# Performance work log

Hardware: AMD Instinct MI355X
Metric: run time of the kernel (lower is better)

Reference implementation:

```python
import jax, jax.numpy as jnp
import numpy as np

WIN = (16, 9, 9)
WIN_SIZE = WIN[0] * WIN[1] * WIN[2]  # 1296
EPS = float(np.e ** -15)             # ~3.06e-7, matches np.power(np.e, -15)


def setup_inputs() -> dict:
    key = jax.random.key(0)
    k1, k2 = jax.random.split(key)
    shape = (2, 1, 96, 192, 192)  # [B, 1, D, H, W]
    I = jax.random.normal(k1, shape, dtype=jnp.float32)
    J = jax.random.normal(k2, shape, dtype=jnp.float32)
    return {"I": I, "J": J}


def _box_sums(tmp):
    # Grouped conv3d with an all-ones [5,1,16,9,9] kernel: per-channel sliding
    k = jnp.ones((5, 1) + WIN, dtype=tmp.dtype)
    return jax.lax.conv_general_dilated(
        tmp, k,
        window_strides=(1, 1, 1),
        padding=[(0, 0), (WIN[1] // 2, WIN[1] // 2), (WIN[2] // 2, WIN[2] // 2)],
        feature_group_count=5,
        dimension_numbers=("NCDHW", "OIDHW", "NCDHW"),
    )


def reference(I, J):
    # I, J: [B, 1, D, H, W]
    tmp = jnp.concatenate([I, J, I * I, J * J, I * J], axis=1)  # [B,5,D,H,W]
    sums = _box_sums(tmp)  # [B, 5, D-15, H, W]
    I_sum, J_sum = sums[:, 0], sums[:, 1]
    I2_sum, J2_sum, IJ_sum = sums[:, 2], sums[:, 3], sums[:, 4]

    u_I = I_sum / WIN_SIZE
    u_J = J_sum / WIN_SIZE

    cross = IJ_sum - u_J * I_sum - u_I * J_sum + u_I * u_J * WIN_SIZE
    I_var = I2_sum - 2.0 * u_I * I_sum + u_I * u_I * WIN_SIZE
    J_var = J2_sum - 2.0 * u_J * J_sum + u_J * u_J * WIN_SIZE

    nz = (I_var * J_var) > EPS  # bool_non_zero; where false, substitute 1.0
    cross = jnp.where(nz, cross, 1.0)
    I_var = jnp.where(nz, I_var, 1.0)
    J_var = jnp.where(nz, J_var, 1.0)

    cc = cross * cross / (I_var * J_var + EPS)  # [B, D-15, H, W]
    loss = -1.0 * jnp.mean(cc, axis=(1, 2, 3)) + 1.0  # [B]
    return loss, cc
```

## Files before the change

### kernel.cpp

```cpp
#include <hip/hip_runtime.h>


constexpr int N = 2, D = 96, H = 192, W = 192;
constexpr int OD = 81;
constexpr int KD = 16;
constexpr int HWp = H * W;
constexpr float INV_WIN = 1.0f / 1296.0f;
constexpr float EPS_NZ = 3.0590232050182579e-07f;
constexpr int CH = 24;
constexpr int ODPB = 14;

__device__ __forceinline__ unsigned bf16rne(float f) {
  unsigned u = __float_as_uint(f);
  return (u + 0x7fffu + ((u >> 16) & 1u)) >> 16;
}
__device__ __forceinline__ float bf16tof(unsigned h) {
  return __uint_as_float(h << 16);
}

__global__ __launch_bounds__(192)
void k_dw(const float* __restrict__ I, const float* __restrict__ J,
          unsigned* __restrict__ ws, int od0, int c, int odcStride) {
  const int h = blockIdx.x;
  const int n = blockIdx.z;
  const int os = od0 + blockIdx.y * ODPB;
  int oe = od0 + c; if (os + ODPB < oe) oe = os + ODPB;
  if (os >= oe) return;
  const int w = threadIdx.x;

  __shared__ float4 x4[2][W + 8];
  __shared__ float  x1[2][W + 8];
  __shared__ float4 a4[2][W + 8];
  __shared__ float  a1[2][W + 8];

  if (w < 4) {
    x4[0][w] = make_float4(0.f,0.f,0.f,0.f); x1[0][w] = 0.f;
    x4[1][w] = make_float4(0.f,0.f,0.f,0.f); x1[1][w] = 0.f;
  }
  if (w >= W - 4) {
    x4[0][w + 8] = make_float4(0.f,0.f,0.f,0.f); x1[0][w + 8] = 0.f;
    x4[1][w + 8] = make_float4(0.f,0.f,0.f,0.f); x1[1][w + 8] = 0.f;
  }
  __syncthreads();

  const size_t colBase = ((size_t)n * D * H + h) * (size_t)W + w;
  const float* Ip = I + colBase;
  const float* Jp = J + colBase;
  unsigned* wbase = ws + ((size_t)n * odcStride * HWp + (size_t)h * W + w) * 3;

  int pe = -1;
  if (w < 3) pe = w + 1;
  else if (w >= W - 3) pe = w + 7;

  const int dEnd = oe + KD - 1;
  float sI = 0.f, sJ = 0.f, sII = 0.f, sJJ = 0.f, sIJ = 0.f;
  float ivN = Ip[(size_t)os * HWp];
  float jvN = Jp[(size_t)os * HWp];
  float ioN = 0.f, joN = 0.f;

  for (int d = os; d < dEnd; ++d) {
    const float iv = ivN, jv = jvN;
    const float io = ioN, jo = joN;
    const int dn = d + 1;
    if (dn < dEnd) {
      ivN = Ip[(size_t)dn * HWp];
      jvN = Jp[(size_t)dn * HWp];
      if (dn >= os + KD - 1) {
        const int odn = dn - (KD - 1);
        ioN = Ip[(size_t)odn * HWp];
        joN = Jp[(size_t)odn * HWp];
      }
    }
    sI += iv; sJ += jv;
    sII += iv * iv; sJJ += jv * jv; sIJ += iv * jv;
    if (d >= os + KD - 1) {
      const int od = d - (KD - 1);
      const int b = d & 1;
      const int p = 4 + w;
      x4[b][p] = make_float4(sI, sJ, sII, sJJ); x1[b][p] = sIJ;
      asm volatile("s_waitcnt lgkmcnt(0)" ::: "memory");
      __builtin_amdgcn_s_barrier();
      {
        float4 m0 = x4[b][p - 1], m1 = x4[b][p], m2 = x4[b][p + 1];
        a4[b][p] = make_float4(m0.x + m1.x + m2.x, m0.y + m1.y + m2.y,
                               m0.z + m1.z + m2.z, m0.w + m1.w + m2.w);
        a1[b][p] = x1[b][p - 1] + x1[b][p] + x1[b][p + 1];
        if (pe >= 0) {
          float4 e0 = x4[b][pe - 1], e1 = x4[b][pe], e2 = x4[b][pe + 1];
          a4[b][pe] = make_float4(e0.x + e1.x + e2.x, e0.y + e1.y + e2.y,
                                  e0.z + e1.z + e2.z, e0.w + e1.w + e2.w);
          a1[b][pe] = x1[b][pe - 1] + x1[b][pe] + x1[b][pe + 1];
        }
      }
      asm volatile("s_waitcnt lgkmcnt(0)" ::: "memory");
      __builtin_amdgcn_s_barrier();
      float4 b0 = a4[b][p - 3], b1 = a4[b][p], b2 = a4[b][p + 3];
      const float r0 = b0.x + b1.x + b2.x;
      const float r1 = b0.y + b1.y + b2.y;
      const float r2 = b0.z + b1.z + b2.z;
      const float r3 = b0.w + b1.w + b2.w;
      const float r4 = a1[b][p - 3] + a1[b][p] + a1[b][p + 3];
      unsigned* o = wbase + (size_t)(od - od0) * HWp * 3;
      uint3 v = make_uint3(bf16rne(r0) | (bf16rne(r1) << 16),
                           bf16rne(r2) | (bf16rne(r3) << 16),
                           bf16rne(r4));
      *(uint3*)o = v;
      sI -= io; sJ -= jo;
      sII -= io * io; sJJ -= jo * jo; sIJ -= io * jo;
    }
  }
}

__global__ __launch_bounds__(192)
void k_hcc(const unsigned* __restrict__ ws, float* __restrict__ cc,
           float* __restrict__ acc, int od0, int odcStride) {
  const int odi = blockIdx.x;
  const int od = od0 + odi;
  const int h0 = blockIdx.y * CH;
  const int n = blockIdx.z;
  const int w = threadIdx.x;
  const unsigned* base =
      ws + ((size_t)n * odcStride * HWp + (size_t)odi * HWp + w) * 3;
  float* ccp = cc + ((size_t)n * OD + od) * (size_t)HWp + w;

  float s0 = 0.f, s1 = 0.f, s2 = 0.f, s3 = 0.f, s4 = 0.f;
  float lsum = 0.f;
  uint3 hist[8];
  const uint3 z3 = make_uint3(0u, 0u, 0u);

  uint3 vN = z3;
  {
    const int hin = h0 - 4;
    if (hin >= 0) vN = *(const uint3*)(base + (size_t)hin * W * 3);
  }
#pragma unroll
  for (int t = 0; t < CH + 8; ++t) {
    const uint3 v = vN;
    if (t + 1 < CH + 8) {
      const int hn = h0 - 4 + t + 1;
      vN = (hn >= 0 && hn < H) ? *(const uint3*)(base + (size_t)hn * W * 3) : z3;
    }
    s0 += bf16tof(v.x & 0xffffu); s1 += bf16tof(v.x >> 16);
    s2 += bf16tof(v.y & 0xffffu); s3 += bf16tof(v.y >> 16);
    s4 += bf16tof(v.z & 0xffffu);
    if (t >= 8) {
      const int h = h0 + t - 8;
      const float cross = s4 - s0 * s1 * INV_WIN;
      const float vI = s2 - s0 * s0 * INV_WIN;
      const float vJ = s3 - s1 * s1 * INV_WIN;
      const float prod = vI * vJ;
      const float c = (prod > EPS_NZ) ? (cross * cross) / (prod + EPS_NZ)
                                      : 1.0f / (1.0f + EPS_NZ);
      ccp[(size_t)h * W] = c;
      lsum += c;
      const uint3 q = hist[t & 7];
      s0 -= bf16tof(q.x & 0xffffu); s1 -= bf16tof(q.x >> 16);
      s2 -= bf16tof(q.y & 0xffffu); s3 -= bf16tof(q.y >> 16);
      s4 -= bf16tof(q.z & 0xffffu);
    }
    hist[t & 7] = v;
  }
  __shared__ float red[3];
#pragma unroll
  for (int off = 32; off > 0; off >>= 1) lsum += __shfl_xor(lsum, off, 64);
  if ((threadIdx.x & 63) == 0) red[threadIdx.x >> 6] = lsum;
  __syncthreads();
  if (threadIdx.x == 0) atomicAdd(acc + n, red[0] + red[1] + red[2]);
}

__global__ void k_fin(const float* __restrict__ acc, float* __restrict__ out) {
  if (threadIdx.x < N)
    out[threadIdx.x] = 1.0f - acc[threadIdx.x] * (1.0f / 2985984.0f);
}

extern "C" void kernel_launch(void* const* d_in, const int* in_sizes, int n_in,
                              void* d_out, int out_size, void* d_ws,
                              size_t ws_size, hipStream_t stream) {
  const float* I = (const float*)d_in[0];
  const float* J = (const float*)d_in[1];
  float* out = (float*)d_out;
  float* acc = (float*)d_ws;
  unsigned* planes = (unsigned*)((char*)d_ws + 256);

  hipMemsetAsync(d_ws, 0, 2 * sizeof(float), stream);

  const size_t perOdPerN = (size_t)HWp * 12;
  size_t avail = (ws_size > 256) ? (ws_size - 256) : 0;
  long long odcMax = (long long)(avail / (2 * perOdPerN));
  if (odcMax < 1) odcMax = 1;
  if (odcMax > OD) odcMax = OD;
  const int odc = (int)odcMax;

  float* ccOut = out + 2;
  for (int od0 = 0; od0 < OD; od0 += odc) {
    const int c = (odc < OD - od0) ? odc : (OD - od0);
    const int S = (c + ODPB - 1) / ODPB;
    hipLaunchKernelGGL(k_dw, dim3(H, S, N), dim3(192), 0, stream,
                       I, J, planes, od0, c, odc);
    hipLaunchKernelGGL(k_hcc, dim3(c, H / CH, N), dim3(192), 0, stream,
                       planes, ccOut, acc, od0, odc);
  }
  hipLaunchKernelGGL(k_fin, dim3(1), dim3(64), 0, stream, acc, out);
}
```

Baseline: 73.29 us.

## Process two H rows per block and prefetch depth loads two steps ahead

The depth/width box-sum kernel now handles two adjacent H rows per block, so each barrier pair is shared across two rows and the grid is halved. It separates the 15-plane warm-up from the steady-state loop and uses a double-buffered register prefetch of entering and leaving planes two output depths ahead, to hide global load latency. The cost is more registers and shared memory per block and fewer blocks in flight, which may reduce occupancy.

```diff
diff --git a/kernel.cpp b/kernel.cpp
--- a/kernel.cpp
+++ b/kernel.cpp
@@ -21,94 +21,123 @@
 __global__ __launch_bounds__(192)
 void k_dw(const float* __restrict__ I, const float* __restrict__ J,
           unsigned* __restrict__ ws, int od0, int c, int odcStride) {
-  const int h = blockIdx.x;
+  const int hA = 2 * blockIdx.x, hB = hA + 1;
   const int n = blockIdx.z;
   const int os = od0 + blockIdx.y * ODPB;
   int oe = od0 + c; if (os + ODPB < oe) oe = os + ODPB;
   if (os >= oe) return;
   const int w = threadIdx.x;
 
-  __shared__ float4 x4[2][W + 8];
-  __shared__ float  x1[2][W + 8];
-  __shared__ float4 a4[2][W + 8];
-  __shared__ float  a1[2][W + 8];
+  __shared__ float4 xA4[W + 8]; __shared__ float xA1[W + 8];
+  __shared__ float4 xB4[W + 8]; __shared__ float xB1[W + 8];
+  __shared__ float4 aA4[W + 8]; __shared__ float aA1[W + 8];
+  __shared__ float4 aB4[W + 8]; __shared__ float aB1[W + 8];
 
   if (w < 4) {
-    x4[0][w] = make_float4(0.f,0.f,0.f,0.f); x1[0][w] = 0.f;
-    x4[1][w] = make_float4(0.f,0.f,0.f,0.f); x1[1][w] = 0.f;
+    xA4[w] = make_float4(0.f,0.f,0.f,0.f); xA1[w] = 0.f;
+    xB4[w] = make_float4(0.f,0.f,0.f,0.f); xB1[w] = 0.f;
   }
   if (w >= W - 4) {
-    x4[0][w + 8] = make_float4(0.f,0.f,0.f,0.f); x1[0][w + 8] = 0.f;
-    x4[1][w + 8] = make_float4(0.f,0.f,0.f,0.f); x1[1][w + 8] = 0.f;
+    xA4[w + 8] = make_float4(0.f,0.f,0.f,0.f); xA1[w + 8] = 0.f;
+    xB4[w + 8] = make_float4(0.f,0.f,0.f,0.f); xB1[w + 8] = 0.f;
   }
   __syncthreads();
 
-  const size_t colBase = ((size_t)n * D * H + h) * (size_t)W + w;
-  const float* Ip = I + colBase;
-  const float* Jp = J + colBase;
-  unsigned* wbase = ws + ((size_t)n * odcStride * HWp + (size_t)h * W + w) * 3;
+  const size_t baseA = ((size_t)n * D * H + hA) * (size_t)W + w;
+  const float* IpA = I + baseA;
+  const float* JpA = J + baseA;
+  const float* IpB = IpA + W;
+  const float* JpB = JpA + W;
+  unsigned* wbA = ws + ((size_t)n * odcStride * HWp + (size_t)hA * W + w) * 3;
+  unsigned* wbB = wbA + (size_t)W * 3;
 
   int pe = -1;
   if (w < 3) pe = w + 1;
   else if (w >= W - 3) pe = w + 7;
-
-  const int dEnd = oe + KD - 1;
-  float sI = 0.f, sJ = 0.f, sII = 0.f, sJJ = 0.f, sIJ = 0.f;
-  float ivN = Ip[(size_t)os * HWp];
-  float jvN = Jp[(size_t)os * HWp];
-  float ioN = 0.f, joN = 0.f;
-
-  for (int d = os; d < dEnd; ++d) {
-    const float iv = ivN, jv = jvN;
-    const float io = ioN, jo = joN;
-    const int dn = d + 1;
-    if (dn < dEnd) {
-      ivN = Ip[(size_t)dn * HWp];
-      jvN = Jp[(size_t)dn * HWp];
-      if (dn >= os + KD - 1) {
-        const int odn = dn - (KD - 1);
-        ioN = Ip[(size_t)odn * HWp];
-        joN = Jp[(size_t)odn * HWp];
-      }
+  const int p = 4 + w;
+
+  float sIA=0.f,sJA=0.f,sIIA=0.f,sJJA=0.f,sIJA=0.f;
+  float sIB=0.f,sJB=0.f,sIIB=0.f,sJJB=0.f,sIJB=0.f;
+  for (int d = os; d < os + KD - 1; ++d) {
+    const float ia = IpA[(size_t)d * HWp], ja = JpA[(size_t)d * HWp];
+    const float ib = IpB[(size_t)d * HWp], jb = JpB[(size_t)d * HWp];
+    sIA += ia; sJA += ja; sIIA += ia*ia; sJJA += ja*ja; sIJA += ia*ja;
+    sIB += ib; sJB += jb; sIIB += ib*ib; sJJB += jb*jb; sIJB += ib*jb;
+  }
+
+#define ISSUE(eIA,eJA,lIA,lJA,eIB,eJB,lIB,lJB, ODX)                          \
+  { const int _o = (ODX);                                                    \
+    eIA = IpA[(size_t)(_o + KD - 1) * HWp];                                  \
+    eJA = JpA[(size_t)(_o + KD - 1) * HWp];                                  \
+    lIA = IpA[(size_t)_o * HWp];                                             \
+    lJA = JpA[(size_t)_o * HWp];                                             \
+    eIB = IpB[(size_t)(_o + KD - 1) * HWp];                                  \
+    eJB = JpB[(size_t)(_o + KD - 1) * HWp];                                  \
+    lIB = IpB[(size_t)_o * HWp];                                             \
+    lJB = JpB[(size_t)_o * HWp]; }
+
+#define COMPUTE(ODX, eIA,eJA,lIA,lJA,eIB,eJB,lIB,lJB)                        \
+  { const int _od = (ODX);                                                   \
+    sIA += eIA; sJA += eJA; sIIA += eIA*eIA; sJJA += eJA*eJA; sIJA += eIA*eJA;\
+    xA4[p] = make_float4(sIA, sJA, sIIA, sJJA); xA1[p] = sIJA;               \
+    sIA -= lIA; sJA -= lJA; sIIA -= lIA*lIA; sJJA -= lJA*lJA; sIJA -= lIA*lJA;\
+    sIB += eIB; sJB += eJB; sIIB += eIB*eIB; sJJB += eJB*eJB; sIJB += eIB*eJB;\
+    xB4[p] = make_float4(sIB, sJB, sIIB, sJJB); xB1[p] = sIJB;               \
+    sIB -= lIB; sJB -= lJB; sIIB -= lIB*lIB; sJJB -= lJB*lJB; sIJB -= lIB*lJB;\
+    asm volatile("s_waitcnt lgkmcnt(0)" ::: "memory");                       \
+    __builtin_amdgcn_s_barrier();                         \
+    { float4 m0 = xA4[p-1], m1 = xA4[p], m2 = xA4[p+1];                      \
+      aA4[p] = make_float4(m0.x+m1.x+m2.x, m0.y+m1.y+m2.y,                   \
+                           m0.z+m1.z+m2.z, m0.w+m1.w+m2.w);                  \
+      aA1[p] = xA1[p-1] + xA1[p] + xA1[p+1];                                 \
+      float4 n0 = xB4[p-1], n1 = xB4[p], n2 = xB4[p+1];                      \
+      aB4[p] = make_float4(n0.x+n1.x+n2.x, n0.y+n1.y+n2.y,                   \
+                           n0.z+n1.z+n2.z, n0.w+n1.w+n2.w);                  \
+      aB1[p] = xB1[p-1] + xB1[p] + xB1[p+1];                                 \
+      if (pe >= 0) {                                                         \
+        float4 e0 = xA4[pe-1], e1 = xA4[pe], e2 = xA4[pe+1];                 \
+        aA4[pe] = make_float4(e0.x+e1.x+e2.x, e0.y+e1.y+e2.y,                \
+                              e0.z+e1.z+e2.z, e0.w+e1.w+e2.w);               \
+        aA1[pe] = xA1[pe-1] + xA1[pe] + xA1[pe+1];                           \
+        float4 f0 = xB4[pe-1], f1 = xB4[pe], f2 = xB4[pe+1];                 \
+        aB4[pe] = make_float4(f0.x+f1.x+f2.x, f0.y+f1.y+f2.y,                \
+                              f0.z+f1.z+f2.z, f0.w+f1.w+f2.w);               \
+        aB1[pe] = xB1[pe-1] + xB1[pe] + xB1[pe+1];                           \
+      } }                                                                    \
+    asm volatile("s_waitcnt lgkmcnt(0)" ::: "memory");                       \
+    __builtin_amdgcn_s_barrier();                         \
+    { float4 b0 = aA4[p-3], b1 = aA4[p], b2 = aA4[p+3];                      \
+      const float r0 = b0.x+b1.x+b2.x, r1 = b0.y+b1.y+b2.y;                  \
+      const float r2 = b0.z+b1.z+b2.z, r3 = b0.w+b1.w+b2.w;                  \
+      const float r4 = aA1[p-3] + aA1[p] + aA1[p+3];                         \
+      unsigned* o = wbA + (size_t)(_od - od0) * HWp * 3;                     \
+      *(uint3*)o = make_uint3(bf16rne(r0) | (bf16rne(r1) << 16),             \
+                              bf16rne(r2) | (bf16rne(r3) << 16),             \
+                              bf16rne(r4));                                  \
+      float4 c0 = aB4[p-3], c1 = aB4[p], c2 = aB4[p+3];                      \
+      const float q0 = c0.x+c1.x+c2.x, q1 = c0.y+c1.y+c2.y;                  \
+      const float q2 = c0.z+c1.z+c2.z, q3 = c0.w+c1.w+c2.w;                  \
+      const float q4 = aB1[p-3] + aB1[p] + aB1[p+3];                         \
+      unsigned* o2 = wbB + (size_t)(_od - od0) * HWp * 3;                    \
+      *(uint3*)o2 = make_uint3(bf16rne(q0) | (bf16rne(q1) << 16),            \
+                               bf16rne(q2) | (bf16rne(q3) << 16),            \
+                               bf16rne(q4)); } }
+
+  float eIA0=0,eJA0=0,lIA0=0,lJA0=0,eIB0=0,eJB0=0,lIB0=0,lJB0=0;
+  float eIA1=0,eJA1=0,lIA1=0,lJA1=0,eIB1=0,eJB1=0,lIB1=0,lJB1=0;
+  ISSUE(eIA0,eJA0,lIA0,lJA0,eIB0,eJB0,lIB0,lJB0, os)
+  if (os + 1 < oe) ISSUE(eIA1,eJA1,lIA1,lJA1,eIB1,eJB1,lIB1,lJB1, os + 1)
+
+  for (int od = os; od < oe; od += 2) {
+    COMPUTE(od, eIA0,eJA0,lIA0,lJA0,eIB0,eJB0,lIB0,lJB0)
+    if (od + 2 < oe) ISSUE(eIA0,eJA0,lIA0,lJA0,eIB0,eJB0,lIB0,lJB0, od + 2)
+    if (od + 1 < oe) {
+      COMPUTE(od + 1, eIA1,eJA1,lIA1,lJA1,eIB1,eJB1,lIB1,lJB1)
+      if (od + 3 < oe) ISSUE(eIA1,eJA1,lIA1,lJA1,eIB1,eJB1,lIB1,lJB1, od + 3)
     }
-    sI += iv; sJ += jv;
-    sII += iv * iv; sJJ += jv * jv; sIJ += iv * jv;
-    if (d >= os + KD - 1) {
-      const int od = d - (KD - 1);
-      const int b = d & 1;
-      const int p = 4 + w;
-      x4[b][p] = make_float4(sI, sJ, sII, sJJ); x1[b][p] = sIJ;
-      asm volatile("s_waitcnt lgkmcnt(0)" ::: "memory");
-      __builtin_amdgcn_s_barrier();
-      {
-        float4 m0 = x4[b][p - 1], m1 = x4[b][p], m2 = x4[b][p + 1];
-        a4[b][p] = make_float4(m0.x + m1.x + m2.x, m0.y + m1.y + m2.y,
-                               m0.z + m1.z + m2.z, m0.w + m1.w + m2.w);
-        a1[b][p] = x1[b][p - 1] + x1[b][p] + x1[b][p + 1];
-        if (pe >= 0) {
-          float4 e0 = x4[b][pe - 1], e1 = x4[b][pe], e2 = x4[b][pe + 1];
-          a4[b][pe] = make_float4(e0.x + e1.x + e2.x, e0.y + e1.y + e2.y,
-                                  e0.z + e1.z + e2.z, e0.w + e1.w + e2.w);
-          a1[b][pe] = x1[b][pe - 1] + x1[b][pe] + x1[b][pe + 1];
-        }
-      }
-      asm volatile("s_waitcnt lgkmcnt(0)" ::: "memory");
-      __builtin_amdgcn_s_barrier();
-      float4 b0 = a4[b][p - 3], b1 = a4[b][p], b2 = a4[b][p + 3];
-      const float r0 = b0.x + b1.x + b2.x;
-      const float r1 = b0.y + b1.y + b2.y;
-      const float r2 = b0.z + b1.z + b2.z;
-      const float r3 = b0.w + b1.w + b2.w;
-      const float r4 = a1[b][p - 3] + a1[b][p] + a1[b][p + 3];
-      unsigned* o = wbase + (size_t)(od - od0) * HWp * 3;
-      uint3 v = make_uint3(bf16rne(r0) | (bf16rne(r1) << 16),
-                           bf16rne(r2) | (bf16rne(r3) << 16),
-                           bf16rne(r4));
-      *(uint3*)o = v;
-      sI -= io; sJ -= jo;
-      sII -= io * io; sJJ -= jo * jo; sIJ -= io * jo;
-    }
-  }
+  }
+#undef ISSUE
+#undef COMPUTE
 }
 
 __global__ __launch_bounds__(192)
@@ -195,7 +224,7 @@
   for (int od0 = 0; od0 < OD; od0 += odc) {
     const int c = (odc < OD - od0) ? odc : (OD - od0);
     const int S = (c + ODPB - 1) / ODPB;
-    hipLaunchKernelGGL(k_dw, dim3(H, S, N), dim3(192), 0, stream,
+    hipLaunchKernelGGL(k_dw, dim3(H / 2, S, N), dim3(192), 0, stream,
                        I, J, planes, od0, c, odc);
     hipLaunchKernelGGL(k_hcc, dim3(c, H / CH, N), dim3(192), 0, stream,
                        planes, ccOut, acc, od0, odc);
```

After: 76.60 us. 4.5% more time.

## Process two depth outputs per barrier pair, prefetch deeper, and spread loss atomics

Applied to the files above, without the earlier changes.

The depth sliding-window loop in k_dw now produces two output depths per pair of barriers, using both shared buffers at once. Global loads are issued two steps ahead through a double set of register buffers. The goal is to halve barrier count and hide load latency. The loss accumulation also spreads atomics over 32 slots per batch and reduces them in k_fin, which cuts atomic contention at the cost of more registers and a larger memset.

```diff
diff --git a/kernel.cpp b/kernel.cpp
--- a/kernel.cpp
+++ b/kernel.cpp
@@ -51,64 +51,113 @@
   int pe = -1;
   if (w < 3) pe = w + 1;
   else if (w >= W - 3) pe = w + 7;
-
-  const int dEnd = oe + KD - 1;
+  const int p = 4 + w;
+
   float sI = 0.f, sJ = 0.f, sII = 0.f, sJJ = 0.f, sIJ = 0.f;
-  float ivN = Ip[(size_t)os * HWp];
-  float jvN = Jp[(size_t)os * HWp];
-  float ioN = 0.f, joN = 0.f;
-
-  for (int d = os; d < dEnd; ++d) {
-    const float iv = ivN, jv = jvN;
-    const float io = ioN, jo = joN;
-    const int dn = d + 1;
-    if (dn < dEnd) {
-      ivN = Ip[(size_t)dn * HWp];
-      jvN = Jp[(size_t)dn * HWp];
-      if (dn >= os + KD - 1) {
-        const int odn = dn - (KD - 1);
-        ioN = Ip[(size_t)odn * HWp];
-        joN = Jp[(size_t)odn * HWp];
-      }
-    }
+  for (int d = os; d < os + KD - 1; ++d) {
+    const float iv = Ip[(size_t)d * HWp];
+    const float jv = Jp[(size_t)d * HWp];
     sI += iv; sJ += jv;
     sII += iv * iv; sJJ += jv * jv; sIJ += iv * jv;
-    if (d >= os + KD - 1) {
-      const int od = d - (KD - 1);
-      const int b = d & 1;
-      const int p = 4 + w;
-      x4[b][p] = make_float4(sI, sJ, sII, sJJ); x1[b][p] = sIJ;
-      asm volatile("s_waitcnt lgkmcnt(0)" ::: "memory");
-      __builtin_amdgcn_s_barrier();
-      {
-        float4 m0 = x4[b][p - 1], m1 = x4[b][p], m2 = x4[b][p + 1];
-        a4[b][p] = make_float4(m0.x + m1.x + m2.x, m0.y + m1.y + m2.y,
-                               m0.z + m1.z + m2.z, m0.w + m1.w + m2.w);
-        a1[b][p] = x1[b][p - 1] + x1[b][p] + x1[b][p + 1];
-        if (pe >= 0) {
-          float4 e0 = x4[b][pe - 1], e1 = x4[b][pe], e2 = x4[b][pe + 1];
-          a4[b][pe] = make_float4(e0.x + e1.x + e2.x, e0.y + e1.y + e2.y,
-                                  e0.z + e1.z + e2.z, e0.w + e1.w + e2.w);
-          a1[b][pe] = x1[b][pe - 1] + x1[b][pe] + x1[b][pe + 1];
-        }
-      }
-      asm volatile("s_waitcnt lgkmcnt(0)" ::: "memory");
-      __builtin_amdgcn_s_barrier();
-      float4 b0 = a4[b][p - 3], b1 = a4[b][p], b2 = a4[b][p + 3];
-      const float r0 = b0.x + b1.x + b2.x;
-      const float r1 = b0.y + b1.y + b2.y;
-      const float r2 = b0.z + b1.z + b2.z;
-      const float r3 = b0.w + b1.w + b2.w;
-      const float r4 = a1[b][p - 3] + a1[b][p] + a1[b][p + 3];
-      unsigned* o = wbase + (size_t)(od - od0) * HWp * 3;
-      uint3 v = make_uint3(bf16rne(r0) | (bf16rne(r1) << 16),
-                           bf16rne(r2) | (bf16rne(r3) << 16),
-                           bf16rne(r4));
-      *(uint3*)o = v;
-      sI -= io; sJ -= jo;
-      sII -= io * io; sJJ -= jo * jo; sIJ -= io * jo;
+  }
+
+#define ISSUE(eA,fA,gA,hA_,eB,fB,gB,hB_, O)                                  \
+  { const int _o = (O);                                                      \
+    if (_o < oe) {                                                           \
+      eA = Ip[(size_t)(_o + KD - 1) * HWp];                                  \
+      fA = Jp[(size_t)(_o + KD - 1) * HWp];                                  \
+      gA = Ip[(size_t)_o * HWp];                                             \
+      hA_ = Jp[(size_t)_o * HWp];                                            \
+      if (_o + 1 < oe) {                                                     \
+        eB = Ip[(size_t)(_o + KD) * HWp];                                    \
+        fB = Jp[(size_t)(_o + KD) * HWp];                                    \
+        gB = Ip[(size_t)(_o + 1) * HWp];                                     \
+        hB_ = Jp[(size_t)(_o + 1) * HWp];                                    \
+      } } }
+
+#define COMPUTE(O, eA,fA,gA,hA_,eB,fB,gB,hB_)                                \
+  { const int _od = (O);                                                     \
+    const bool two = (_od + 1 < oe);                                         \
+    sI += eA; sJ += fA;                                                      \
+    sII += eA * eA; sJJ += fA * fA; sIJ += eA * fA;                          \
+    x4[0][p] = make_float4(sI, sJ, sII, sJJ); x1[0][p] = sIJ;                \
+    sI -= gA; sJ -= hA_;                                                     \
+    sII -= gA * gA; sJJ -= hA_ * hA_; sIJ -= gA * hA_;                       \
+    if (two) {                                                               \
+      sI += eB; sJ += fB;                                                    \
+      sII += eB * eB; sJJ += fB * fB; sIJ += eB * fB;                        \
+      x4[1][p] = make_float4(sI, sJ, sII, sJJ); x1[1][p] = sIJ;              \
+      sI -= gB; sJ -= hB_;                                                   \
+      sII -= gB * gB; sJJ -= hB_ * hB_; sIJ -= gB * hB_;                     \
+    }                                                                        \
+    asm volatile("s_waitcnt lgkmcnt(0)" ::: "memory");                       \
+    __builtin_amdgcn_s_barrier();                         \
+    {                                                                        \
+      float4 m0 = x4[0][p - 1], m1 = x4[0][p], m2 = x4[0][p + 1];            \
+      a4[0][p] = make_float4(m0.x + m1.x + m2.x, m0.y + m1.y + m2.y,         \
+                             m0.z + m1.z + m2.z, m0.w + m1.w + m2.w);        \
+      a1[0][p] = x1[0][p - 1] + x1[0][p] + x1[0][p + 1];                     \
+      if (pe >= 0) {                                                         \
+        float4 e0 = x4[0][pe - 1], e1 = x4[0][pe], e2 = x4[0][pe + 1];       \
+        a4[0][pe] = make_float4(e0.x + e1.x + e2.x, e0.y + e1.y + e2.y,      \
+                                e0.z + e1.z + e2.z, e0.w + e1.w + e2.w);     \
+        a1[0][pe] = x1[0][pe - 1] + x1[0][pe] + x1[0][pe + 1];               \
+      }                                                                      \
+    }                                                                        \
+    if (two) {                                                               \
+      float4 m0 = x4[1][p - 1], m1 = x4[1][p], m2 = x4[1][p + 1];            \
+      a4[1][p] = make_float4(m0.x + m1.x + m2.x, m0.y + m1.y + m2.y,         \
+                             m0.z + m1.z + m2.z, m0.w + m1.w + m2.w);        \
+      a1[1][p] = x1[1][p - 1] + x1[1][p] + x1[1][p + 1];                     \
+      if (pe >= 0) {                                                         \
+        float4 e0 = x4[1][pe - 1], e1 = x4[1][pe], e2 = x4[1][pe + 1];       \
+        a4[1][pe] = make_float4(e0.x + e1.x + e2.x, e0.y + e1.y + e2.y,      \
+                                e0.z + e1.z + e2.z, e0.w + e1.w + e2.w);     \
+        a1[1][pe] = x1[1][pe - 1] + x1[1][pe] + x1[1][pe + 1];               \
+      }                                                                      \
+    }                                                                        \
+    asm volatile("s_waitcnt lgkmcnt(0)" ::: "memory");                       \
+    __builtin_amdgcn_s_barrier();                         \
+    {                                                                        \
+      float4 b0 = a4[0][p - 3], b1 = a4[0][p], b2 = a4[0][p + 3];            \
+      const float r0 = b0.x + b1.x + b2.x;                                   \
+      const float r1 = b0.y + b1.y + b2.y;                                   \
+      const float r2 = b0.z + b1.z + b2.z;                                   \
+      const float r3 = b0.w + b1.w + b2.w;                                   \
+      const float r4 = a1[0][p - 3] + a1[0][p] + a1[0][p + 3];               \
+      unsigned* o = wbase + (size_t)(_od - od0) * HWp * 3;                   \
+      *(uint3*)o = make_uint3(bf16rne(r0) | (bf16rne(r1) << 16),             \
+                              bf16rne(r2) | (bf16rne(r3) << 16),             \
+                              bf16rne(r4));                                  \
+    }                                                                        \
+    if (two) {                                                               \
+      float4 b0 = a4[1][p - 3], b1 = a4[1][p], b2 = a4[1][p + 3];            \
+      const float r0 = b0.x + b1.x + b2.x;                                   \
+      const float r1 = b0.y + b1.y + b2.y;                                   \
+      const float r2 = b0.z + b1.z + b2.z;                                   \
+      const float r3 = b0.w + b1.w + b2.w;                                   \
+      const float r4 = a1[1][p - 3] + a1[1][p] + a1[1][p + 3];               \
+      unsigned* o = wbase + (size_t)(_od + 1 - od0) * HWp * 3;               \
+      *(uint3*)o = make_uint3(bf16rne(r0) | (bf16rne(r1) << 16),             \
+                              bf16rne(r2) | (bf16rne(r3) << 16),             \
+                              bf16rne(r4));                                  \
+    } }
+
+  float eA0=0,fA0=0,gA0=0,hA0=0, eA1=0,fA1=0,gA1=0,hA1=0;
+  float eB0=0,fB0=0,gB0=0,hB0=0, eB1=0,fB1=0,gB1=0,hB1=0;
+  ISSUE(eA0,fA0,gA0,hA0,eA1,fA1,gA1,hA1, os)
+  ISSUE(eB0,fB0,gB0,hB0,eB1,fB1,gB1,hB1, os + 2)
+
+  for (int od = os; od < oe; od += 4) {
+    COMPUTE(od, eA0,fA0,gA0,hA0,eA1,fA1,gA1,hA1)
+    ISSUE(eA0,fA0,gA0,hA0,eA1,fA1,gA1,hA1, od + 4)
+    if (od + 2 < oe) {
+      COMPUTE(od + 2, eB0,fB0,gB0,hB0,eB1,fB1,gB1,hB1)
+      ISSUE(eB0,fB0,gB0,hB0,eB1,fB1,gB1,hB1, od + 6)
     }
   }
+#undef ISSUE
+#undef COMPUTE
 }
 
 __global__ __launch_bounds__(192)
@@ -165,12 +214,17 @@
   for (int off = 32; off > 0; off >>= 1) lsum += __shfl_xor(lsum, off, 64);
   if ((threadIdx.x & 63) == 0) red[threadIdx.x >> 6] = lsum;
   __syncthreads();
-  if (threadIdx.x == 0) atomicAdd(acc + n, red[0] + red[1] + red[2]);
+  if (threadIdx.x == 0)
+    atomicAdd(acc + n * 32 + (odi & 31), red[0] + red[1] + red[2]);
 }
 
 __global__ void k_fin(const float* __restrict__ acc, float* __restrict__ out) {
-  if (threadIdx.x < N)
-    out[threadIdx.x] = 1.0f - acc[threadIdx.x] * (1.0f / 2985984.0f);
+  const int t = threadIdx.x;
+  float v = acc[t];
+#pragma unroll
+  for (int off = 16; off > 0; off >>= 1) v += __shfl_xor(v, off, 32);
+  if (t == 0)  out[0] = 1.0f - v * (1.0f / 2985984.0f);
+  if (t == 32) out[1] = 1.0f - v * (1.0f / 2985984.0f);
 }
 
 extern "C" void kernel_launch(void* const* d_in, const int* in_sizes, int n_in,
@@ -182,7 +236,7 @@
   float* acc = (float*)d_ws;
   unsigned* planes = (unsigned*)((char*)d_ws + 256);
 
-  hipMemsetAsync(d_ws, 0, 2 * sizeof(float), stream);
+  hipMemsetAsync(d_ws, 0, 64 * sizeof(float), stream);
 
   const size_t perOdPerN = (size_t)HWp * 12;
   size_t avail = (ws_size > 256) ? (ws_size - 256) : 0;
```

Result: faster. 64.42 us, median of 5 (-12.1%).
